# Kernel tuning notes

Measured on AMD Instinct MI355X. Metric: run time of the kernel, lower is better.

The kernel has to match this reference:

```python
import jax, jax.numpy as jnp
import numpy as np

NOISE_STD = 0.1
TOP_K = 2

def setup_inputs() -> dict:
    key = jax.random.key(0)
    k1, k2, k3, k4 = jax.random.split(key, 4)
    B, S, H = 4, 4096, 2048
    E, SE, NS = 64, 64, 10
    x = jax.random.normal(k1, (B, S, H), dtype=jnp.float32)
    scale_embeddings = jax.random.normal(k2, (NS, SE), dtype=jnp.float32)
    # nn.Linear(H+SE, E, bias=False) weight: [E, H+SE]
    router_w = jax.random.normal(k3, (E, H + SE), dtype=jnp.float32) / np.sqrt(H + SE).astype(np.float32)
    # pre-sampled standard-normal noise (training path), scaled by NOISE_STD inside reference
    noise = jax.random.normal(k4, (B, S, E), dtype=jnp.float32)
    return {"x": x, "scale_embeddings": scale_embeddings, "router_w": router_w,
            "noise": noise, "scale_idx": 3}

def reference(x, scale_embeddings, router_w, noise, scale_idx):
    B, S, _ = x.shape
    # scale_idx is not None branch: lookup one scale embedding, broadcast over tokens
    emb = scale_embeddings[scale_idx]                      # [SE]
    emb = jnp.broadcast_to(emb, (B, S, emb.shape[-1]))     # [B,S,SE]
    x_with_scale = jnp.concatenate([x, emb], axis=-1)      # [B,S,H+SE]
    # router: bias-free linear projection to expert logits
    router_logits = jnp.einsum('bsd,ed->bse', x_with_scale, router_w)
    router_logits = router_logits + noise * NOISE_STD      # training noise injection
    routing_probs = jax.nn.softmax(router_logits, axis=-1)  # [B,S,E]
    routing_weights, selected_experts = jax.lax.top_k(routing_probs, TOP_K)
    routing_weights = routing_weights / routing_weights.sum(axis=-1, keepdims=True)
    # scatter normalized weights into dense dispatch tensor [B,S,E]
    dispatch = (jax.nn.one_hot(selected_experts, routing_probs.shape[-1],
                               dtype=routing_probs.dtype)
                * routing_weights[..., None]).sum(axis=-2)
    return dispatch
```

## Files before the change

### kernel.cpp

```cpp
#include <hip/hip_runtime.h>
#include <hip/hip_bf16.h>
#include <math.h>
#include <stdint.h>


#define H_DIM 2048
#define K_TOTAL 2112
#define E_DIM 64
#define SE_DIM 64
#define NSTEP 64
#define TPB 32
#define NBLOCKS (16384 / TPB)
#define STEP_BYTES (12 * 1024)
#define WP_TOTAL (NSTEP * STEP_BYTES)

typedef float  f32x4 __attribute__((ext_vector_type(4)));
typedef short  s16x8 __attribute__((ext_vector_type(8)));
typedef unsigned int u32x4 __attribute__((ext_vector_type(4)));

typedef uint32_t __attribute__((address_space(1))) gu32_t;
typedef uint32_t __attribute__((address_space(3))) lu32_t;
__device__ __forceinline__ void gload_lds16(const void* g, void* l) {
    __builtin_amdgcn_global_load_lds((const gu32_t*)g, (lu32_t*)l, 16, 0, 0);
}

__device__ __forceinline__ unsigned short bf16_rne(float f) {
    uint32_t u = __float_as_uint(f);
    return (unsigned short)((u + 0x7FFFu + ((u >> 16) & 1u)) >> 16);
}
__device__ __forceinline__ float bf16_f32(unsigned short h) {
    return __uint_as_float(((uint32_t)h) << 16);
}
__device__ __forceinline__ uint32_t bits_of_bf2(__hip_bfloat162 h) {
    uint32_t u; __builtin_memcpy(&u, &h, 4); return u;
}

__global__ void prep_kernel(const float* __restrict__ W,
                            const float* __restrict__ se,
                            const int* __restrict__ sidx,
                            unsigned short* __restrict__ Wp,
                            float* __restrict__ tail) {
    if (blockIdx.x == 64) {
        int e = threadIdx.x;
        if (e < 64) {
            const float* emb = se + (*sidx) * SE_DIM;
            float t = 0.f;
            for (int j = 0; j < SE_DIM; ++j)
                t = fmaf(emb[j], W[(size_t)e * K_TOTAL + H_DIM + j], t);
            tail[e] = t;
        }
        return;
    }
    int item = blockIdx.x * 256 + threadIdx.x;
    int lane = item & 63;
    int nt   = (item >> 6) & 3;
    int s    = item >> 8;
    int e     = nt * 16 + (lane & 15);
    int kbase = s * 32 + (lane >> 4) * 8;
    const float* wr = W + (size_t)e * K_TOTAL + kbase;
    unsigned short p0[8], p1[8], p2[8];
    #pragma unroll
    for (int j = 0; j < 8; ++j) {
        float v = wr[j];
        unsigned short a0 = bf16_rne(v);
        float r1 = v - bf16_f32(a0);
        unsigned short a1 = bf16_rne(r1);
        float r2 = r1 - bf16_f32(a1);
        p0[j] = a0; p1[j] = a1; p2[j] = bf16_rne(r2);
    }
    size_t rec = (size_t)s * 12 + nt * 3;
    unsigned short* d0 = Wp + (rec + 0) * 512 + lane * 8;
    unsigned short* d1 = Wp + (rec + 1) * 512 + lane * 8;
    unsigned short* d2 = Wp + (rec + 2) * 512 + lane * 8;
    #pragma unroll
    for (int j = 0; j < 8; ++j) { d0[j] = p0[j]; d1[j] = p1[j]; d2[j] = p2[j]; }
}

__device__ __forceinline__ void split3(const float4 fa, const float4 fb,
                                       s16x8& P0, s16x8& P1, s16x8& P2) {
    float f[8] = {fa.x, fa.y, fa.z, fa.w, fb.x, fb.y, fb.z, fb.w};
    uint32_t d0[4], d1[4], d2[4];
    #pragma unroll
    for (int p = 0; p < 4; ++p) {
        float v0 = f[2 * p], v1 = f[2 * p + 1];
        uint32_t u0 = bits_of_bf2(__float22bfloat162_rn(make_float2(v0, v1)));
        float r0 = v0 - __uint_as_float(u0 << 16);
        float r1 = v1 - __uint_as_float(u0 & 0xffff0000u);
        uint32_t u1 = bits_of_bf2(__float22bfloat162_rn(make_float2(r0, r1)));
        float s0 = r0 - __uint_as_float(u1 << 16);
        float s1 = r1 - __uint_as_float(u1 & 0xffff0000u);
        uint32_t u2 = bits_of_bf2(__float22bfloat162_rn(make_float2(s0, s1)));
        d0[p] = u0; d1[p] = u1; d2[p] = u2;
    }
    u32x4 q0 = {d0[0], d0[1], d0[2], d0[3]};
    u32x4 q1 = {d1[0], d1[1], d1[2], d1[3]};
    u32x4 q2 = {d2[0], d2[1], d2[2], d2[3]};
    __builtin_memcpy(&P0, &q0, 16);
    __builtin_memcpy(&P1, &q1, 16);
    __builtin_memcpy(&P2, &q2, 16);
}

__launch_bounds__(256, 2)
__global__ void router_kernel(const float* __restrict__ x,
                              const unsigned char* __restrict__ Wp,
                              const float* __restrict__ tail_g,
                              const float* __restrict__ noise,
                              float* __restrict__ out) {
    __shared__ __align__(16) unsigned char bb[2][STEP_BYTES];
    __shared__ float4 cand2[2][TPB];
    __shared__ float4 res[TPB];

    const int tid  = threadIdx.x;
    const int lane = tid & 63;
    const int wave = __builtin_amdgcn_readfirstlane(tid >> 6);
    const int mt   = wave >> 1;
    const int g    = wave & 1;
    const int tok0 = blockIdx.x * TPB;
    const int row  = lane & 15;
    const int quad = lane >> 4;
    const int c    = row;

    const float* aptr = x + (size_t)(tok0 + mt * 16 + row) * H_DIM + quad * 8;

    f32x4 acc0 = {0.f, 0.f, 0.f, 0.f}, acc1 = acc0;

    #pragma unroll
    for (int i = 0; i < 3; ++i) {
        int f = tid + i * 256;
        gload_lds16(Wp + f * 16, &bb[0][f * 16]);
    }

    for (int s = 0; s < NSTEP; ++s) {
        __syncthreads();
        if (s + 1 < NSTEP) {
            const unsigned char* src = Wp + (size_t)(s + 1) * STEP_BYTES;
            #pragma unroll
            for (int i = 0; i < 3; ++i) {
                int f = tid + i * 256;
                gload_lds16(src + f * 16, &bb[(s + 1) & 1][f * 16]);
            }
        }
        const float* ap = aptr + (size_t)s * 32;
        float4 a0 = *(const float4*)(ap);
        float4 a1 = *(const float4*)(ap + 4);
        s16x8 A0, A1, A2;
        split3(a0, a1, A0, A1, A2);

        const unsigned char* base = &bb[s & 1][g * 6144 + lane * 16];
        #pragma unroll
        for (int nt = 0; nt < 2; ++nt) {
            s16x8 B0 = *(const s16x8*)(base + (nt * 3 + 0) * 1024);
            s16x8 B1 = *(const s16x8*)(base + (nt * 3 + 1) * 1024);
            s16x8 B2 = *(const s16x8*)(base + (nt * 3 + 2) * 1024);
            f32x4 a = nt ? acc1 : acc0;
            a = __builtin_amdgcn_mfma_f32_16x16x32_bf16(A0, B0, a, 0, 0, 0);
            a = __builtin_amdgcn_mfma_f32_16x16x32_bf16(A0, B1, a, 0, 0, 0);
            a = __builtin_amdgcn_mfma_f32_16x16x32_bf16(A1, B0, a, 0, 0, 0);
            a = __builtin_amdgcn_mfma_f32_16x16x32_bf16(A0, B2, a, 0, 0, 0);
            a = __builtin_amdgcn_mfma_f32_16x16x32_bf16(A1, B1, a, 0, 0, 0);
            a = __builtin_amdgcn_mfma_f32_16x16x32_bf16(A2, B0, a, 0, 0, 0);
            if (nt) acc1 = a; else acc0 = a;
        }
    }

    float tl0 = tail_g[g * 32 + c], tl1 = tail_g[g * 32 + 16 + c];
    #pragma unroll
    for (int r = 0; r < 4; ++r) {
        const int tl = mt * 16 + quad * 4 + r;
        const float* nz = noise + (size_t)(tok0 + tl) * E_DIM + g * 32;
        float v0 = acc0[r] + tl0 + 0.1f * nz[c];
        float v1 = acc1[r] + tl1 + 0.1f * nz[16 + c];
        float V1, V2; int I1, I2;
        if (v1 > v0) { V1 = v1; I1 = g * 32 + 16 + c; V2 = v0; I2 = g * 32 + c; }
        else         { V1 = v0; I1 = g * 32 + c;      V2 = v1; I2 = g * 32 + 16 + c; }
        #pragma unroll
        for (int m = 8; m; m >>= 1) {
            float o1 = __shfl_xor(V1, m, 64); int oi1 = __shfl_xor(I1, m, 64);
            float o2 = __shfl_xor(V2, m, 64); int oi2 = __shfl_xor(I2, m, 64);
            if (o1 > V1 || (o1 == V1 && oi1 < I1)) {
                float nv2; int ni2;
                if (V1 > o2 || (V1 == o2 && I1 < oi2)) { nv2 = V1; ni2 = I1; }
                else                                   { nv2 = o2; ni2 = oi2; }
                V1 = o1; I1 = oi1; V2 = nv2; I2 = ni2;
            } else {
                if (o1 > V2 || (o1 == V2 && oi1 < I2)) { V2 = o1; I2 = oi1; }
            }
        }
        if (c == r)
            cand2[g][tl] = make_float4(V1, __int_as_float(I1), V2, __int_as_float(I2));
    }
    __syncthreads();

    if (tid < TPB) {
        float4 c0 = cand2[0][tid];
        float4 c1 = cand2[1][tid];
        float V1 = c0.x, V2 = c0.z;
        int   I1 = __float_as_int(c0.y), I2 = __float_as_int(c0.w);
        if (c1.x > V1) {
            if (c1.z > V1) { V2 = c1.z; I2 = __float_as_int(c1.w); }
            else           { V2 = V1;   I2 = I1; }
            V1 = c1.x; I1 = __float_as_int(c1.y);
        } else if (c1.x > V2) {
            V2 = c1.x; I2 = __float_as_int(c1.y);
        }
        float d   = expf(V2 - V1);
        float inv = 1.0f / (1.0f + d);
        res[tid] = make_float4(inv, __int_as_float(I1), d * inv, __int_as_float(I2));
    }
    __syncthreads();

    float4* outb = (float4*)out + (size_t)blockIdx.x * (TPB * E_DIM / 4);
    #pragma unroll
    for (int pp = 0; pp < 2; ++pp) {
        int p = tid + pp * 256;
        int t = p >> 4, cc = p & 15;
        float4 rr = res[t];
        int ri1 = __float_as_int(rr.y), ri2 = __float_as_int(rr.w);
        int e = cc * 4;
        float4 o;
        o.x = (e + 0 == ri1) ? rr.x : (e + 0 == ri2) ? rr.z : 0.0f;
        o.y = (e + 1 == ri1) ? rr.x : (e + 1 == ri2) ? rr.z : 0.0f;
        o.z = (e + 2 == ri1) ? rr.x : (e + 2 == ri2) ? rr.z : 0.0f;
        o.w = (e + 3 == ri1) ? rr.x : (e + 3 == ri2) ? rr.z : 0.0f;
        outb[p] = o;
    }
}

extern "C" void kernel_launch(void* const* d_in, const int* in_sizes, int n_in,
                              void* d_out, int out_size, void* d_ws, size_t ws_size,
                              hipStream_t stream) {
    const float* x     = (const float*)d_in[0];
    const float* se    = (const float*)d_in[1];
    const float* W     = (const float*)d_in[2];
    const float* noise = (const float*)d_in[3];
    const int*   sidx  = (const int*)d_in[4];
    float* out = (float*)d_out;

    unsigned short* Wp   = (unsigned short*)d_ws;
    float*          tail = (float*)((char*)d_ws + WP_TOTAL);

    hipLaunchKernelGGL(prep_kernel, dim3(65), dim3(256), 0, stream, W, se, sidx, Wp, tail);
    hipLaunchKernelGGL(router_kernel, dim3(NBLOCKS), dim3(256), 0, stream,
                       x, (const unsigned char*)Wp, tail, noise, out);
}
```

Baseline: 243.1 us.

## Load router weights directly into registers with software-pipelined prefetch

Drops the LDS double-buffer of the packed weight slices and the per-step __syncthreads. Each wave now reads its weight fragments straight from global memory (expected to hit in L2) into registers, two steps ahead, and reads activations up to four steps ahead through a 4-way unrolled rotating-register pipeline. The goal is to remove the barrier and LDS round-trip costs and get deeper prefetch of x. In exchange it raises register pressure and repeats weight loads per wave through the cache hierarchy.

```diff
diff --git a/kernel.cpp b/kernel.cpp
--- a/kernel.cpp
+++ b/kernel.cpp
@@ -13,16 +13,11 @@
 #define NBLOCKS (16384 / TPB)
 #define STEP_BYTES (12 * 1024)
 #define WP_TOTAL (NSTEP * STEP_BYTES)
+#define MINS(v) ((v) < NSTEP ? (v) : (NSTEP - 1))
 
 typedef float  f32x4 __attribute__((ext_vector_type(4)));
 typedef short  s16x8 __attribute__((ext_vector_type(8)));
 typedef unsigned int u32x4 __attribute__((ext_vector_type(4)));
-
-typedef uint32_t __attribute__((address_space(1))) gu32_t;
-typedef uint32_t __attribute__((address_space(3))) lu32_t;
-__device__ __forceinline__ void gload_lds16(const void* g, void* l) {
-    __builtin_amdgcn_global_load_lds((const gu32_t*)g, (lu32_t*)l, 16, 0, 0);
-}
 
 __device__ __forceinline__ unsigned short bf16_rne(float f) {
     uint32_t u = __float_as_uint(f);
@@ -100,13 +95,47 @@
     __builtin_memcpy(&P2, &q2, 16);
 }
 
+#define LDB(r0, r1, r2, r3, r4, r5, sidx) do {                          \
+    const char* _p = bptr + (size_t)(sidx) * STEP_BYTES;                \
+    r0 = *(const uint4*)(_p);                                           \
+    r1 = *(const uint4*)(_p + 1024);                                    \
+    r2 = *(const uint4*)(_p + 2048);                                    \
+    r3 = *(const uint4*)(_p + 3072);                                    \
+    r4 = *(const uint4*)(_p + 4096);                                    \
+    r5 = *(const uint4*)(_p + 5120);                                    \
+} while (0)
+
+#define LDA(da, db, sidx) do {                                          \
+    const float* _a = aptr + (size_t)(sidx) * 32;                       \
+    da = *(const float4*)(_a);                                          \
+    db = *(const float4*)(_a + 4);                                      \
+} while (0)
+
+#define MFMA6(A0, A1, A2, b0, b1, b2, accv) do {                              \
+    accv = __builtin_amdgcn_mfma_f32_16x16x32_bf16(A0, b0, accv, 0, 0, 0);    \
+    accv = __builtin_amdgcn_mfma_f32_16x16x32_bf16(A0, b1, accv, 0, 0, 0);    \
+    accv = __builtin_amdgcn_mfma_f32_16x16x32_bf16(A1, b0, accv, 0, 0, 0);    \
+    accv = __builtin_amdgcn_mfma_f32_16x16x32_bf16(A0, b2, accv, 0, 0, 0);    \
+    accv = __builtin_amdgcn_mfma_f32_16x16x32_bf16(A1, b1, accv, 0, 0, 0);    \
+    accv = __builtin_amdgcn_mfma_f32_16x16x32_bf16(A2, b0, accv, 0, 0, 0);    \
+} while (0)
+
+#define COMPUTE(Aa, Ab, r0, r1, r2, r3, r4, r5) do {                    \
+    s16x8 A0, A1, A2; split3(Aa, Ab, A0, A1, A2);                       \
+    s16x8 b0, b1, b2, b3, b4, b5;                                       \
+    __builtin_memcpy(&b0, &r0, 16); __builtin_memcpy(&b1, &r1, 16);     \
+    __builtin_memcpy(&b2, &r2, 16); __builtin_memcpy(&b3, &r3, 16);     \
+    __builtin_memcpy(&b4, &r4, 16); __builtin_memcpy(&b5, &r5, 16);     \
+    MFMA6(A0, A1, A2, b0, b1, b2, acc0);                                \
+    MFMA6(A0, A1, A2, b3, b4, b5, acc1);                                \
+} while (0)
+
 __launch_bounds__(256, 2)
 __global__ void router_kernel(const float* __restrict__ x,
                               const unsigned char* __restrict__ Wp,
                               const float* __restrict__ tail_g,
                               const float* __restrict__ noise,
                               float* __restrict__ out) {
-    __shared__ __align__(16) unsigned char bb[2][STEP_BYTES];
     __shared__ float4 cand2[2][TPB];
     __shared__ float4 res[TPB];
 
@@ -121,46 +150,30 @@
     const int c    = row;
 
     const float* aptr = x + (size_t)(tok0 + mt * 16 + row) * H_DIM + quad * 8;
+    const char* bptr = (const char*)Wp + g * 6144 + lane * 16;
 
     f32x4 acc0 = {0.f, 0.f, 0.f, 0.f}, acc1 = acc0;
 
-    #pragma unroll
-    for (int i = 0; i < 3; ++i) {
-        int f = tid + i * 256;
-        gload_lds16(Wp + f * 16, &bb[0][f * 16]);
-    }
-
-    for (int s = 0; s < NSTEP; ++s) {
-        __syncthreads();
-        if (s + 1 < NSTEP) {
-            const unsigned char* src = Wp + (size_t)(s + 1) * STEP_BYTES;
-            #pragma unroll
-            for (int i = 0; i < 3; ++i) {
-                int f = tid + i * 256;
-                gload_lds16(src + f * 16, &bb[(s + 1) & 1][f * 16]);
-            }
-        }
-        const float* ap = aptr + (size_t)s * 32;
-        float4 a0 = *(const float4*)(ap);
-        float4 a1 = *(const float4*)(ap + 4);
-        s16x8 A0, A1, A2;
-        split3(a0, a1, A0, A1, A2);
-
-        const unsigned char* base = &bb[s & 1][g * 6144 + lane * 16];
-        #pragma unroll
-        for (int nt = 0; nt < 2; ++nt) {
-            s16x8 B0 = *(const s16x8*)(base + (nt * 3 + 0) * 1024);
-            s16x8 B1 = *(const s16x8*)(base + (nt * 3 + 1) * 1024);
-            s16x8 B2 = *(const s16x8*)(base + (nt * 3 + 2) * 1024);
-            f32x4 a = nt ? acc1 : acc0;
-            a = __builtin_amdgcn_mfma_f32_16x16x32_bf16(A0, B0, a, 0, 0, 0);
-            a = __builtin_amdgcn_mfma_f32_16x16x32_bf16(A0, B1, a, 0, 0, 0);
-            a = __builtin_amdgcn_mfma_f32_16x16x32_bf16(A1, B0, a, 0, 0, 0);
-            a = __builtin_amdgcn_mfma_f32_16x16x32_bf16(A0, B2, a, 0, 0, 0);
-            a = __builtin_amdgcn_mfma_f32_16x16x32_bf16(A1, B1, a, 0, 0, 0);
-            a = __builtin_amdgcn_mfma_f32_16x16x32_bf16(A2, B0, a, 0, 0, 0);
-            if (nt) acc1 = a; else acc0 = a;
-        }
+    float4 A0a, A0b, A1a, A1b, A2a, A2b, A3a, A3b;
+    uint4 c0, c1, c2, c3, c4, c5;
+    uint4 n0, n1, n2, n3, n4, n5;
+    LDA(A0a, A0b, 0); LDA(A1a, A1b, 1); LDA(A2a, A2b, 2); LDA(A3a, A3b, 3);
+    LDB(c0, c1, c2, c3, c4, c5, 0);
+    LDB(n0, n1, n2, n3, n4, n5, 1);
+
+    for (int sb = 0; sb < NSTEP; sb += 4) {
+        COMPUTE(A0a, A0b, c0, c1, c2, c3, c4, c5);
+        LDA(A0a, A0b, MINS(sb + 4));
+        LDB(c0, c1, c2, c3, c4, c5, MINS(sb + 2));
+        COMPUTE(A1a, A1b, n0, n1, n2, n3, n4, n5);
+        LDA(A1a, A1b, MINS(sb + 5));
+        LDB(n0, n1, n2, n3, n4, n5, MINS(sb + 3));
+        COMPUTE(A2a, A2b, c0, c1, c2, c3, c4, c5);
+        LDA(A2a, A2b, MINS(sb + 6));
+        LDB(c0, c1, c2, c3, c4, c5, MINS(sb + 4));
+        COMPUTE(A3a, A3b, n0, n1, n2, n3, n4, n5);
+        LDA(A3a, A3b, MINS(sb + 7));
+        LDB(n0, n1, n2, n3, n4, n5, MINS(sb + 5));
     }
 
     float tl0 = tail_g[g * 32 + c], tl1 = tail_g[g * 32 + 16 + c];
@@ -192,16 +205,16 @@
     __syncthreads();
 
     if (tid < TPB) {
-        float4 c0 = cand2[0][tid];
-        float4 c1 = cand2[1][tid];
-        float V1 = c0.x, V2 = c0.z;
-        int   I1 = __float_as_int(c0.y), I2 = __float_as_int(c0.w);
-        if (c1.x > V1) {
-            if (c1.z > V1) { V2 = c1.z; I2 = __float_as_int(c1.w); }
+        float4 q0 = cand2[0][tid];
+        float4 q1 = cand2[1][tid];
+        float V1 = q0.x, V2 = q0.z;
+        int   I1 = __float_as_int(q0.y), I2 = __float_as_int(q0.w);
+        if (q1.x > V1) {
+            if (q1.z > V1) { V2 = q1.z; I2 = __float_as_int(q1.w); }
             else           { V2 = V1;   I2 = I1; }
-            V1 = c1.x; I1 = __float_as_int(c1.y);
-        } else if (c1.x > V2) {
-            V2 = c1.x; I2 = __float_as_int(c1.y);
+            V1 = q1.x; I1 = __float_as_int(q1.y);
+        } else if (q1.x > V2) {
+            V2 = q1.x; I2 = __float_as_int(q1.y);
         }
         float d   = expf(V2 - V1);
         float inv = 1.0f / (1.0f + d);
```

Measured after the change: 300.3 us. 23.5% more time.

## Stage activations through LDS with a four-slot async pipeline

Applied to the files above, without the earlier changes.

Activation tiles now travel from global memory into swizzled LDS through async global_load_lds, like the weights, instead of being read from global straight into registers. The weight buffer grows from two slots to four, with three steps issued ahead. The per-step __syncthreads becomes an explicit s_waitcnt vmcnt(8) plus barrier, so loads for later steps stay in flight during compute. This adds LDS footprint (about 64KB per block), which may limit occupancy, and the fixed vmcnt count depends on exactly four loads per step.

```diff
diff --git a/kernel.cpp b/kernel.cpp
--- a/kernel.cpp
+++ b/kernel.cpp
@@ -13,6 +13,7 @@
 #define NBLOCKS (16384 / TPB)
 #define STEP_BYTES (12 * 1024)
 #define WP_TOTAL (NSTEP * STEP_BYTES)
+#define MINS(v) ((v) < NSTEP ? (v) : (NSTEP - 1))
 
 typedef float  f32x4 __attribute__((ext_vector_type(4)));
 typedef short  s16x8 __attribute__((ext_vector_type(8)));
@@ -106,7 +107,8 @@
                               const float* __restrict__ tail_g,
                               const float* __restrict__ noise,
                               float* __restrict__ out) {
-    __shared__ __align__(16) unsigned char bb[2][STEP_BYTES];
+    __shared__ __align__(16) unsigned char As[4][4096];
+    __shared__ __align__(16) unsigned char Bs[4][STEP_BYTES];
     __shared__ float4 cand2[2][TPB];
     __shared__ float4 res[TPB];
 
@@ -120,33 +122,40 @@
     const int quad = lane >> 4;
     const int c    = row;
 
-    const float* aptr = x + (size_t)(tok0 + mt * 16 + row) * H_DIM + quad * 8;
+    const int stok = tid >> 3;
+    const int spos = tid & 7;
+    const int schk = spos ^ (stok & 7);
+    const float* asrc = x + (size_t)(tok0 + stok) * H_DIM + schk * 4;
+
+    const int abase = (mt * 16 + row) * 128;
+    const int aoff0 = abase + (((quad * 2)     ^ (row & 7)) << 4);
+    const int aoff1 = abase + (((quad * 2 + 1) ^ (row & 7)) << 4);
 
     f32x4 acc0 = {0.f, 0.f, 0.f, 0.f}, acc1 = acc0;
 
-    #pragma unroll
-    for (int i = 0; i < 3; ++i) {
-        int f = tid + i * 256;
-        gload_lds16(Wp + f * 16, &bb[0][f * 16]);
-    }
+    #define ISSUE_SET(s_, d_) do {                                          \
+        const unsigned char* _bsrc = Wp + (size_t)(s_) * STEP_BYTES;        \
+        gload_lds16(asrc + (size_t)(s_) * 32, &As[d_][tid * 16]);           \
+        gload_lds16(_bsrc + (size_t)tid * 16,          &Bs[d_][tid * 16]);          \
+        gload_lds16(_bsrc + (size_t)(tid + 256) * 16,  &Bs[d_][(tid + 256) * 16]);  \
+        gload_lds16(_bsrc + (size_t)(tid + 512) * 16,  &Bs[d_][(tid + 512) * 16]);  \
+    } while (0)
+
+    ISSUE_SET(0, 0);
+    ISSUE_SET(1, 1);
+    ISSUE_SET(2, 2);
 
     for (int s = 0; s < NSTEP; ++s) {
-        __syncthreads();
-        if (s + 1 < NSTEP) {
-            const unsigned char* src = Wp + (size_t)(s + 1) * STEP_BYTES;
-            #pragma unroll
-            for (int i = 0; i < 3; ++i) {
-                int f = tid + i * 256;
-                gload_lds16(src + f * 16, &bb[(s + 1) & 1][f * 16]);
-            }
-        }
-        const float* ap = aptr + (size_t)s * 32;
-        float4 a0 = *(const float4*)(ap);
-        float4 a1 = *(const float4*)(ap + 4);
+        asm volatile("s_waitcnt vmcnt(8)\n\ts_barrier" ::: "memory");
+
+        const int slot = s & 3;
+        const float4* ab = (const float4*)&As[slot][0];
+        float4 a0 = *(const float4*)((const unsigned char*)ab + aoff0);
+        float4 a1 = *(const float4*)((const unsigned char*)ab + aoff1);
         s16x8 A0, A1, A2;
         split3(a0, a1, A0, A1, A2);
 
-        const unsigned char* base = &bb[s & 1][g * 6144 + lane * 16];
+        const unsigned char* base = &Bs[slot][g * 6144 + lane * 16];
         #pragma unroll
         for (int nt = 0; nt < 2; ++nt) {
             s16x8 B0 = *(const s16x8*)(base + (nt * 3 + 0) * 1024);
@@ -161,7 +170,10 @@
             a = __builtin_amdgcn_mfma_f32_16x16x32_bf16(A2, B0, a, 0, 0, 0);
             if (nt) acc1 = a; else acc0 = a;
         }
-    }
+
+        ISSUE_SET(MINS(s + 3), (s + 3) & 3);
+    }
+    #undef ISSUE_SET
 
     float tl0 = tail_g[g * 32 + c], tl1 = tail_g[g * 32 + 16 + c];
     #pragma unroll
@@ -192,16 +204,16 @@
     __syncthreads();
 
     if (tid < TPB) {
-        float4 c0 = cand2[0][tid];
-        float4 c1 = cand2[1][tid];
-        float V1 = c0.x, V2 = c0.z;
-        int   I1 = __float_as_int(c0.y), I2 = __float_as_int(c0.w);
-        if (c1.x > V1) {
-            if (c1.z > V1) { V2 = c1.z; I2 = __float_as_int(c1.w); }
+        float4 q0 = cand2[0][tid];
+        float4 q1 = cand2[1][tid];
+        float V1 = q0.x, V2 = q0.z;
+        int   I1 = __float_as_int(q0.y), I2 = __float_as_int(q0.w);
+        if (q1.x > V1) {
+            if (q1.z > V1) { V2 = q1.z; I2 = __float_as_int(q1.w); }
             else           { V2 = V1;   I2 = I1; }
-            V1 = c1.x; I1 = __float_as_int(c1.y);
-        } else if (c1.x > V2) {
-            V2 = c1.x; I2 = __float_as_int(c1.y);
+            V1 = q1.x; I1 = __float_as_int(q1.y);
+        } else if (q1.x > V2) {
+            V2 = q1.x; I2 = __float_as_int(q1.y);
         }
         float d   = expf(V2 - V1);
         float inv = 1.0f / (1.0f + d);
```

Measured after the change: 222.7 us. 1.09x faster.
